# Kernel optimization log

Hardware: AMD Instinct MI355X
Metric: run time of the kernel (lower is better)

The kernel has to match this reference:

```python
import jax, jax.numpy as jnp
import numpy as np

B, N, C = 4, 2048, 1152
H = 16
DH = C // H  # 72
EPS = 1e-6
THETA = 10000.0


def _rms_norm(x, w):
    # per-head RMSNorm in fp32, matching LlamaRMSNorm
    xf = x.astype(jnp.float32)
    var = jnp.mean(xf * xf, axis=-1, keepdims=True)
    return (w * (xf * jax.lax.rsqrt(var + EPS)).astype(x.dtype))


def _rope_cos_sin(n, dh, dtype):
    half = dh // 2
    inv_freq = 1.0 / (THETA ** (jnp.arange(0, half, dtype=jnp.float32) / half))
    ang = jnp.arange(n, dtype=jnp.float32)[:, None] * inv_freq[None, :]  # [N, half]
    return jnp.cos(ang).astype(dtype), jnp.sin(ang).astype(dtype)


def _apply_rope(x, cos, sin):
    # x: [B,H,N,DH]; rotate-half style
    half = x.shape[-1] // 2
    x1, x2 = x[..., :half], x[..., half:]
    return jnp.concatenate([x1 * cos - x2 * sin, x2 * cos + x1 * sin], axis=-1)


def setup_inputs() -> dict:
    key = jax.random.key(0)
    ks = jax.random.split(key, 3)
    x = jax.random.normal(ks[0], (B, N, C), dtype=jnp.float32)
    w_qkv = jax.random.normal(ks[1], (3 * C, C), dtype=jnp.float32) * (C ** -0.5)
    w_proj = jax.random.normal(ks[2], (C, C), dtype=jnp.float32) * (C ** -0.5)
    b_proj = jnp.zeros((C,), dtype=jnp.float32)
    q_norm_w = jnp.ones((DH,), dtype=jnp.float32)
    k_norm_w = jnp.ones((DH,), dtype=jnp.float32)
    return {"x": x, "w_qkv": w_qkv, "w_proj": w_proj, "b_proj": b_proj,
            "q_norm_w": q_norm_w, "k_norm_w": k_norm_w}


def reference(x, w_qkv, w_proj, b_proj, q_norm_w, k_norm_w):
    b, n, c = x.shape
    # QKV projection (no bias)
    qkv = jnp.einsum('bnc,dc->bnd', x, w_qkv)  # [B,N,3C]
    qkv = qkv.reshape(b, n, 3, H, DH).transpose(2, 0, 3, 1, 4)  # [3,B,H,N,DH]
    q, k, v = qkv[0], qkv[1], qkv[2]
    # RoPE on q, k
    cos, sin = _rope_cos_sin(n, DH, x.dtype)  # [N, DH/2]
    q = _apply_rope(q, cos, sin)
    k = _apply_rope(k, cos, sin)
    # per-head QK RMSNorm
    q = _rms_norm(q, q_norm_w)
    k = _rms_norm(k, k_norm_w)
    # scaled dot-product attention
    scale = DH ** -0.5
    attn = jax.nn.softmax(jnp.einsum('bhqd,bhkd->bhqk', q, k) * scale, axis=-1)
    out = jnp.einsum('bhqk,bhkd->bhqd', attn, v)  # [B,H,N,DH]
    out = out.transpose(0, 2, 1, 3).reshape(b, n, c)
    return jnp.einsum('bnc,dc->bnd', out, w_proj) + b_proj
```

## Files before the change

kernel.cpp:

```cpp
#include <hip/hip_runtime.h>
#include <stdint.h>

#define BATCH 4
#define NSEQ  2048
#define CDIM  1152
#define HB    16
#define DHD   72
#define D3    3456
#define NT    8192

typedef __attribute__((ext_vector_type(8))) short short8;
typedef __attribute__((ext_vector_type(8))) unsigned short u16x8;
typedef __attribute__((ext_vector_type(4))) unsigned short u16x4;
typedef __attribute__((ext_vector_type(2))) unsigned int u32x2;
typedef __attribute__((ext_vector_type(4))) float f32x4;

__device__ __forceinline__ float bf2f(unsigned short u) {
  return __uint_as_float(((unsigned)u) << 16);
}
__device__ __forceinline__ unsigned short f2bf(float f) {
  unsigned u = __float_as_uint(f);
  u += 0x7FFF + ((u >> 16) & 1);
  return (unsigned short)(u >> 16);
}
__device__ __forceinline__ unsigned pkbf(float lo, float hi) {
  unsigned r;
  asm("v_cvt_pk_bf16_f32 %0, %1, %2" : "=v"(r) : "v"(lo), "v"(hi));
  return r;
}

__device__ __forceinline__ void gload_lds16(const unsigned short* g, unsigned short* l) {
  __builtin_amdgcn_global_load_lds(
      (const __attribute__((address_space(1))) void*)g,
      (__attribute__((address_space(3))) void*)l, 16, 0, 0);
}

#define XN    ((size_t)NT * CDIM)
#define WQN   ((size_t)D3 * CDIM)
#define WPN   ((size_t)CDIM * CDIM)
#define CVT_CHUNKS ((XN + WQN + WPN) / 4)

__global__ __launch_bounds__(256) void cvt_bf16(
    const float* __restrict__ x, const float* __restrict__ wq,
    const float* __restrict__ wp, unsigned short* __restrict__ xb,
    unsigned short* __restrict__ wqb, unsigned short* __restrict__ wpb) {
  size_t c = (size_t)blockIdx.x * 256 + threadIdx.x;
  if (c >= CVT_CHUNKS) return;
  const float* src;
  unsigned short* dst;
  size_t e = c * 4;
  if (e < XN) { src = x + e; dst = xb + e; }
  else if (e < XN + WQN) { src = wq + (e - XN); dst = wqb + (e - XN); }
  else { src = wp + (e - XN - WQN); dst = wpb + (e - XN - WQN); }
  f32x4 v = *(const f32x4*)src;
  u16x4 r;
#pragma unroll
  for (int i = 0; i < 4; i++) r[i] = f2bf(v[i]);
  *(u16x4*)dst = r;
}

template <int SCATTER>
__global__ __launch_bounds__(256) void gemm_bt(
    const unsigned short* __restrict__ A, const unsigned short* __restrict__ Bt,
    const float* __restrict__ bias, void* __restrict__ Cout,
    unsigned short* __restrict__ Vt, int M, int Dn, int K) {
  __shared__ __attribute__((aligned(16))) unsigned short sA[128 * 32];
  __shared__ __attribute__((aligned(16))) unsigned short sB[128 * 32];

  const int tid  = threadIdx.x;
  const int lane = tid & 63;
  const int w    = tid >> 6;
  const int wm   = w >> 1, wn = w & 1;
  const int quad = lane >> 4, l16 = lane & 15;

  const int gx  = gridDim.x;
  const int nwg = gx * gridDim.y;
  const int lb  = blockIdx.y * gx + blockIdx.x;
  const int swz = (lb & 7) * (nwg >> 3) + (lb >> 3);
  const int m0 = (swz / gx) * 128, n0 = (swz % gx) * 128;

  const int srow = (lane >> 2);
  const int scol = (lane & 3) << 3;

  const f32x4 zero = {0.f, 0.f, 0.f, 0.f};
  f32x4 acc[4][4];
#pragma unroll
  for (int i = 0; i < 4; i++)
#pragma unroll
    for (int j = 0; j < 4; j++) acc[i][j] = zero;

  for (int kt = 0; kt < K; kt += 32) {
#pragma unroll
    for (int i = 0; i < 2; i++) {
      int ck = w * 2 + i;
      gload_lds16(A + (size_t)(m0 + ck * 16 + srow) * K + kt + scol, sA + ck * 512);
      gload_lds16(Bt + (size_t)(n0 + ck * 16 + srow) * K + kt + scol, sB + ck * 512);
    }
    __syncthreads();

    short8 a[4], b[4];
#pragma unroll
    for (int i = 0; i < 4; i++)
      a[i] = *(const short8*)(sA + (wm * 64 + i * 16 + l16) * 32 + quad * 8);
#pragma unroll
    for (int j = 0; j < 4; j++)
      b[j] = *(const short8*)(sB + (wn * 64 + j * 16 + l16) * 32 + quad * 8);

#pragma unroll
    for (int i = 0; i < 4; i++)
#pragma unroll
      for (int j = 0; j < 4; j++)
        acc[i][j] = __builtin_amdgcn_mfma_f32_16x16x32_bf16(a[i], b[j], acc[i][j], 0, 0, 0);
    __syncthreads();
  }

#pragma unroll
  for (int i = 0; i < 4; i++) {
    int row = m0 + wm * 64 + i * 16 + quad * 4;
#pragma unroll
    for (int j = 0; j < 4; j++) {
      int col = n0 + wn * 64 + j * 16 + l16;
      if (SCATTER) {
        int s  = col / CDIM;
        int rm = col - s * CDIM;
        int h  = rm / DHD;
        int dh = rm - h * DHD;
        int b_ = row >> 11;
        int n  = row & 2047;
        if (s == 2) {
#pragma unroll
          for (int r = 0; r < 4; r++)
            Vt[((size_t)(b_ * HB + h) * DHD + dh) * NSEQ + n + r] = f2bf(acc[i][j][r]);
        } else {
          unsigned short* Cb = (unsigned short*)Cout;
#pragma unroll
          for (int r = 0; r < 4; r++)
            Cb[(((size_t)(s * BATCH + b_) * HB + h) * NSEQ + (n + r)) * DHD + dh] =
                f2bf(acc[i][j][r]);
        }
      } else {
        float bb = bias ? bias[col] : 0.f;
        float* Cf = (float*)Cout;
#pragma unroll
        for (int r = 0; r < 4; r++)
          Cf[(size_t)(row + r) * Dn + col] = acc[i][j][r] + bb;
      }
    }
  }
}

__global__ __launch_bounds__(256) void rope_rms(
    unsigned short* __restrict__ qkvb,
    const float* __restrict__ qw, const float* __restrict__ kw) {
  const int blk = blockIdx.x;
  const int b = blk >> 11;
  const int n = blk & 2047;
  const int tid = threadIdx.x;

  __shared__ float sv[2][CDIM];
  __shared__ float srsq[2][HB];

  const float nf = (float)n;
  const float l2t_over_half = 13.287712379549449f / 36.0f;
  const float scale2 = 0.17002329230297715f;

  for (int e = tid; e < CDIM; e += 256) {
    int h  = e / DHD;
    int dh = e - h * DHD;
    int i  = (dh < 36) ? dh : dh - 36;
    float inv_freq = exp2f(-l2t_over_half * (float)i);
    float ang = nf * inv_freq;
    float sn, cs;
    __sincosf(ang, &sn, &cs);
#pragma unroll
    for (int sel = 0; sel < 2; sel++) {
      size_t ah = (((size_t)(sel * BATCH + b) * HB + h) * NSEQ + n) * DHD;
      float x1 = bf2f(qkvb[ah + i]);
      float x2 = bf2f(qkvb[ah + i + 36]);
      sv[sel][e] = (dh < 36) ? (x1 * cs - x2 * sn) : (x2 * cs + x1 * sn);
    }
  }
  __syncthreads();
  if (tid < 128) {
    int sel = tid >> 6;
    int h = (tid & 63) >> 2, p = tid & 3;
    float s = 0.f;
#pragma unroll
    for (int d = 0; d < 18; d++) {
      float v = sv[sel][h * DHD + p * 18 + d];
      s += v * v;
    }
    s += __shfl_xor(s, 1);
    s += __shfl_xor(s, 2);
    if (p == 0)
      srsq[sel][h] = rsqrtf(s * (1.0f / 72.0f) + 1e-6f) * (sel ? 1.0f : scale2);
  }
  __syncthreads();
  for (int e = tid; e < CDIM; e += 256) {
    int h  = e / DHD;
    int dh = e - h * DHD;
#pragma unroll
    for (int sel = 0; sel < 2; sel++) {
      const float* wnorm = sel ? kw : qw;
      size_t ah = (((size_t)(sel * BATCH + b) * HB + h) * NSEQ + n) * DHD;
      qkvb[ah + dh] = f2bf(sv[sel][e] * srsq[sel][h] * wnorm[dh]);
    }
  }
}

__global__ __launch_bounds__(256, 4) void flash_attn(
    const unsigned short* __restrict__ qkvb, const unsigned short* __restrict__ Vt,
    unsigned short* __restrict__ AO) {
  __shared__ __attribute__((aligned(16))) unsigned short sK[64 * 72];
  __shared__ __attribute__((aligned(16))) unsigned short sVt[80 * 64];
  __shared__ __attribute__((aligned(16))) unsigned short sP[128 * 64];

  const int tid  = threadIdx.x;
  const int w    = tid >> 6;
  const int lane = tid & 63;
  const int quad = lane >> 4, l16 = lane & 15;
  const int s7   = l16 & 7;
  const int q0 = blockIdx.x * 128;
  const int h = blockIdx.y, b = blockIdx.z;

  const unsigned short* Qb = qkvb + ((size_t)(0 * BATCH + b) * HB + h) * NSEQ * DHD;
  const unsigned short* Kb = qkvb + ((size_t)(1 * BATCH + b) * HB + h) * NSEQ * DHD;
  const unsigned short* Vb = Vt + (size_t)(b * HB + h) * DHD * NSEQ;

  const short8 zs = {0, 0, 0, 0, 0, 0, 0, 0};
  const f32x4 zero = {0.f, 0.f, 0.f, 0.f};

  const int vswz = ((lane & 7) ^ (lane >> 3)) * 8;
  const unsigned short* pKn[3];
  const unsigned short* pVn[3];
#pragma unroll
  for (int j = 0; j < 3; j++) {
    int i = w + 4 * j;
    int ii = (i < 9) ? i : 0;
    pKn[j] = Kb + ii * 512 + lane * 8;
    pVn[j] = Vb + (size_t)(ii * 8 + (lane >> 3)) * NSEQ + vswz;
  }

#pragma unroll
  for (int j = 0; j < 3; j++) {
    int i = w + 4 * j;
    if (i < 9) {
      gload_lds16(pKn[j], sK + i * 512);
      gload_lds16(pVn[j], sVt + i * 512);
      pKn[j] += 64 * 72;
      pVn[j] += 64;
    }
  }

  for (int e = tid; e < 512; e += 256)
    sVt[72 * 64 + e] = (e < 64) ? (unsigned short)0x3F80 : (unsigned short)0;

  short8 aq[2][3];
#pragma unroll
  for (int qt = 0; qt < 2; qt++) {
    const unsigned short* qrow = Qb + (size_t)(q0 + w * 32 + qt * 16 + l16) * DHD;
    aq[qt][0] = *(const short8*)(qrow + quad * 8);
    aq[qt][1] = *(const short8*)(qrow + 32 + quad * 8);
    aq[qt][2] = (quad == 0) ? *(const short8*)(qrow + 64) : zs;
  }

  f32x4 o[2][5];
#pragma unroll
  for (int qt = 0; qt < 2; qt++)
#pragma unroll
    for (int nb = 0; nb < 5; nb++) o[qt][nb] = zero;

  auto sphase_pack = [&]() {
    f32x4 st[2][4];
    __builtin_amdgcn_s_setprio(1);
#pragma unroll
    for (int nk = 0; nk < 4; nk++) {
      const unsigned short* kr = sK + (nk * 16 + l16) * 72;
      short8 kf0 = *(const short8*)(kr + quad * 8);
      short8 kf1 = *(const short8*)(kr + 32 + quad * 8);
      short8 kf2 = *(const short8*)(kr + 64);
      f32x4 s0 = zero, s1 = zero;
      s0 = __builtin_amdgcn_mfma_f32_16x16x32_bf16(kf0, aq[0][0], s0, 0, 0, 0);
      s1 = __builtin_amdgcn_mfma_f32_16x16x32_bf16(kf0, aq[1][0], s1, 0, 0, 0);
      s0 = __builtin_amdgcn_mfma_f32_16x16x32_bf16(kf1, aq[0][1], s0, 0, 0, 0);
      s1 = __builtin_amdgcn_mfma_f32_16x16x32_bf16(kf1, aq[1][1], s1, 0, 0, 0);
      s0 = __builtin_amdgcn_mfma_f32_16x16x32_bf16(kf2, aq[0][2], s0, 0, 0, 0);
      s1 = __builtin_amdgcn_mfma_f32_16x16x32_bf16(kf2, aq[1][2], s1, 0, 0, 0);
      st[0][nk] = s0;
      st[1][nk] = s1;
    }
    __builtin_amdgcn_s_setprio(0);
#pragma unroll
    for (int qt = 0; qt < 2; qt++) {
      unsigned short* prow = sP + (qt * 64 + w * 16 + l16) * 64 + (quad & 1) * 4;
#pragma unroll
      for (int nk = 0; nk < 4; nk++) {
        int uoff = ((nk * 2 + (quad >> 1)) ^ s7) << 3;
        u32x2 pr;
        pr[0] = pkbf(exp2f(st[qt][nk][0]), exp2f(st[qt][nk][1]));
        pr[1] = pkbf(exp2f(st[qt][nk][2]), exp2f(st[qt][nk][3]));
        *(u32x2*)(prow + uoff) = pr;
      }
    }
  };

  auto pv_phase = [&]() {
    __builtin_amdgcn_s_setprio(1);
#pragma unroll
    for (int kb = 0; kb < 2; kb++) {
      const unsigned short* pp =
          sP + (w * 16 + l16) * 64 + (((kb * 4 + quad) ^ s7) << 3);
      short8 pf0 = *(const short8*)pp;
      short8 pf1 = *(const short8*)(pp + 64 * 64);
#pragma unroll
      for (int nb = 0; nb < 5; nb++) {
        short8 vf = *(const short8*)(sVt + (nb * 16 + l16) * 64 +
                                     (((kb * 4 + quad) ^ s7) << 3));
        o[0][nb] = __builtin_amdgcn_mfma_f32_16x16x32_bf16(pf0, vf, o[0][nb], 0, 0, 0);
        o[1][nb] = __builtin_amdgcn_mfma_f32_16x16x32_bf16(pf1, vf, o[1][nb], 0, 0, 0);
      }
    }
    __builtin_amdgcn_s_setprio(0);
  };

  __syncthreads();

  for (int t = 0; t < 32; t++) {
    sphase_pack();

    __syncthreads();

    if (t < 31) {
#pragma unroll
      for (int j = 0; j < 3; j++) {
        int i = w + 4 * j;
        if (i < 9) { gload_lds16(pKn[j], sK + i * 512); pKn[j] += 64 * 72; }
      }
    }

    pv_phase();

    __syncthreads();

    if (t < 31) {
#pragma unroll
      for (int j = 0; j < 3; j++) {
        int i = w + 4 * j;
        if (i < 9) { gload_lds16(pVn[j], sVt + i * 512); pVn[j] += 64; }
      }
    }
  }

#pragma unroll
  for (int qt = 0; qt < 2; qt++) {
    float inv[4];
#pragma unroll
    for (int r = 0; r < 4; r++)
      inv[r] = 1.0f / __shfl(o[qt][4][r], (quad << 4) + 8, 64);
    const int qrow = q0 + w * 32 + qt * 16 + quad * 4;
#pragma unroll
    for (int nb = 0; nb < 5; nb++) {
      int dh = nb * 16 + l16;
      if (dh < DHD) {
#pragma unroll
        for (int r = 0; r < 4; r++)
          AO[((size_t)b * NSEQ + qrow + r) * CDIM + h * DHD + dh] =
              f2bf(o[qt][nb][r] * inv[r]);
      }
    }
  }
}

extern "C" void kernel_launch(void* const* d_in, const int* in_sizes, int n_in,
                              void* d_out, int out_size, void* d_ws, size_t ws_size,
                              hipStream_t stream) {
  const float* x      = (const float*)d_in[0];
  const float* w_qkv  = (const float*)d_in[1];
  const float* w_proj = (const float*)d_in[2];
  const float* b_proj = (const float*)d_in[3];
  const float* qnw    = (const float*)d_in[4];
  const float* knw    = (const float*)d_in[5];
  float* out = (float*)d_out;

  char* ws = (char*)d_ws;
  unsigned short* xb    = (unsigned short*)(ws);
  unsigned short* wqkvb = (unsigned short*)(ws + 18874368);
  unsigned short* wprojb= (unsigned short*)(ws + 26836992);
  unsigned short* qkvb  = (unsigned short*)(ws + 29491200);
  unsigned short* Vt    = (unsigned short*)(ws + 67239936);
  unsigned short* AO    = xb;

  cvt_bf16<<<dim3((CVT_CHUNKS + 255) / 256), 256, 0, stream>>>(
      x, w_qkv, w_proj, xb, wqkvb, wprojb);
  gemm_bt<1><<<dim3(D3 / 128, NT / 128), 256, 0, stream>>>(
      xb, wqkvb, nullptr, qkvb, Vt, NT, D3, CDIM);
  rope_rms<<<dim3(NT), 256, 0, stream>>>(qkvb, qnw, knw);
  flash_attn<<<dim3(NSEQ / 128, HB, BATCH), 256, 0, stream>>>(qkvb, Vt, AO);
  gemm_bt<0><<<dim3(CDIM / 128, NT / 128), 256, 0, stream>>>(
      AO, wprojb, b_proj, out, nullptr, NT, CDIM, CDIM);
}
```

Measured before the change: 393.8 us.

## Deepen GEMM K-tile with XOR-swizzled LDS and vectorize rope_rms memory access

```diff
diff --git a/kernel.cpp b/kernel.cpp
--- a/kernel.cpp
+++ b/kernel.cpp
@@ -64,23 +64,27 @@
     const unsigned short* __restrict__ A, const unsigned short* __restrict__ Bt,
     const float* __restrict__ bias, void* __restrict__ Cout,
     unsigned short* __restrict__ Vt, int M, int Dn, int K) {
-  __shared__ __attribute__((aligned(16))) unsigned short sA[128 * 32];
-  __shared__ __attribute__((aligned(16))) unsigned short sB[128 * 32];
+  __shared__ __attribute__((aligned(16))) unsigned short sA[128 * 64];
+  __shared__ __attribute__((aligned(16))) unsigned short sB[128 * 64];
 
   const int tid  = threadIdx.x;
   const int lane = tid & 63;
   const int w    = tid >> 6;
   const int wm   = w >> 1, wn = w & 1;
   const int quad = lane >> 4, l16 = lane & 15;
+  const int s7l  = l16 & 7;
 
   const int gx  = gridDim.x;
-  const int nwg = gx * gridDim.y;
   const int lb  = blockIdx.y * gx + blockIdx.x;
-  const int swz = (lb & 7) * (nwg >> 3) + (lb >> 3);
-  const int m0 = (swz / gx) * 128, n0 = (swz % gx) * 128;
-
-  const int srow = (lane >> 2);
-  const int scol = (lane & 3) << 3;
+  const int xcd = lb & 7;
+  const int pos = lb >> 3;
+  const int m0 = ((xcd << 3) + (pos & 7)) * 128;
+  const int n0 = (pos >> 3) * 128;
+
+  const int r8 = lane >> 3;
+  const int cu = (lane & 7) ^ r8;
+  const unsigned short* gA = A  + (size_t)(m0 + w * 32 + r8) * K + cu * 8;
+  const unsigned short* gB = Bt + (size_t)(n0 + w * 32 + r8) * K + cu * 8;
 
   const f32x4 zero = {0.f, 0.f, 0.f, 0.f};
   f32x4 acc[4][4];
@@ -89,28 +93,30 @@
 #pragma unroll
     for (int j = 0; j < 4; j++) acc[i][j] = zero;
 
-  for (int kt = 0; kt < K; kt += 32) {
-#pragma unroll
-    for (int i = 0; i < 2; i++) {
-      int ck = w * 2 + i;
-      gload_lds16(A + (size_t)(m0 + ck * 16 + srow) * K + kt + scol, sA + ck * 512);
-      gload_lds16(Bt + (size_t)(n0 + ck * 16 + srow) * K + kt + scol, sB + ck * 512);
+  for (int kt = 0; kt < K; kt += 64) {
+#pragma unroll
+    for (int i = 0; i < 4; i++) {
+      gload_lds16(gA + (size_t)i * 8 * K + kt, sA + (w * 4 + i) * 512);
+      gload_lds16(gB + (size_t)i * 8 * K + kt, sB + (w * 4 + i) * 512);
     }
     __syncthreads();
 
-    short8 a[4], b[4];
-#pragma unroll
-    for (int i = 0; i < 4; i++)
-      a[i] = *(const short8*)(sA + (wm * 64 + i * 16 + l16) * 32 + quad * 8);
-#pragma unroll
-    for (int j = 0; j < 4; j++)
-      b[j] = *(const short8*)(sB + (wn * 64 + j * 16 + l16) * 32 + quad * 8);
-
-#pragma unroll
-    for (int i = 0; i < 4; i++)
-#pragma unroll
-      for (int j = 0; j < 4; j++)
-        acc[i][j] = __builtin_amdgcn_mfma_f32_16x16x32_bf16(a[i], b[j], acc[i][j], 0, 0, 0);
+#pragma unroll
+    for (int kk = 0; kk < 2; kk++) {
+      short8 a[4], b[4];
+#pragma unroll
+      for (int i = 0; i < 4; i++) {
+        a[i] = *(const short8*)(sA + (wm * 64 + i * 16 + l16) * 64 +
+                                (((kk * 4 + quad) ^ s7l) << 3));
+        b[i] = *(const short8*)(sB + (wn * 64 + i * 16 + l16) * 64 +
+                                (((kk * 4 + quad) ^ s7l) << 3));
+      }
+#pragma unroll
+      for (int i = 0; i < 4; i++)
+#pragma unroll
+        for (int j = 0; j < 4; j++)
+          acc[i][j] = __builtin_amdgcn_mfma_f32_16x16x32_bf16(a[i], b[j], acc[i][j], 0, 0, 0);
+    }
     __syncthreads();
   }
 
@@ -164,23 +170,35 @@
   const float l2t_over_half = 13.287712379549449f / 36.0f;
   const float scale2 = 0.17002329230297715f;
 
-  for (int e = tid; e < CDIM; e += 256) {
-    int h  = e / DHD;
-    int dh = e - h * DHD;
-    int i  = (dh < 36) ? dh : dh - 36;
-    float inv_freq = exp2f(-l2t_over_half * (float)i);
-    float ang = nf * inv_freq;
+  for (int g = tid; g < 288; g += 256) {
+    int sel = (g >= 144) ? 1 : 0;
+    int gg  = g - sel * 144;
+    int h   = gg / 9;
+    int u   = gg - h * 9;
+    const unsigned short* src =
+        qkvb + (((size_t)(sel * BATCH + b) * HB + h) * NSEQ + n) * DHD + u * 8;
+    u16x8 v = *(const u16x8*)src;
+    float* dst = &sv[sel][h * DHD + u * 8];
+#pragma unroll
+    for (int r = 0; r < 8; r++) dst[r] = bf2f(v[r]);
+  }
+  __syncthreads();
+
+  for (int p = tid; p < 1152; p += 256) {
+    int sel = (p >= 576) ? 1 : 0;
+    int pp  = p - sel * 576;
+    int h   = pp / 36;
+    int i   = pp - h * 36;
+    float* row = &sv[sel][h * DHD];
+    float x1 = row[i], x2 = row[i + 36];
+    float ang = nf * exp2f(-l2t_over_half * (float)i);
     float sn, cs;
     __sincosf(ang, &sn, &cs);
-#pragma unroll
-    for (int sel = 0; sel < 2; sel++) {
-      size_t ah = (((size_t)(sel * BATCH + b) * HB + h) * NSEQ + n) * DHD;
-      float x1 = bf2f(qkvb[ah + i]);
-      float x2 = bf2f(qkvb[ah + i + 36]);
-      sv[sel][e] = (dh < 36) ? (x1 * cs - x2 * sn) : (x2 * cs + x1 * sn);
-    }
+    row[i]      = x1 * cs - x2 * sn;
+    row[i + 36] = x2 * cs + x1 * sn;
   }
   __syncthreads();
+
   if (tid < 128) {
     int sel = tid >> 6;
     int h = (tid & 63) >> 2, p = tid & 3;
@@ -196,15 +214,21 @@
       srsq[sel][h] = rsqrtf(s * (1.0f / 72.0f) + 1e-6f) * (sel ? 1.0f : scale2);
   }
   __syncthreads();
-  for (int e = tid; e < CDIM; e += 256) {
-    int h  = e / DHD;
-    int dh = e - h * DHD;
-#pragma unroll
-    for (int sel = 0; sel < 2; sel++) {
-      const float* wnorm = sel ? kw : qw;
-      size_t ah = (((size_t)(sel * BATCH + b) * HB + h) * NSEQ + n) * DHD;
-      qkvb[ah + dh] = f2bf(sv[sel][e] * srsq[sel][h] * wnorm[dh]);
-    }
+
+  for (int g = tid; g < 288; g += 256) {
+    int sel = (g >= 144) ? 1 : 0;
+    int gg  = g - sel * 144;
+    int h   = gg / 9;
+    int u   = gg - h * 9;
+    float rs = srsq[sel][h];
+    const float* wn = (sel ? kw : qw) + u * 8;
+    const float* s = &sv[sel][h * DHD + u * 8];
+    u16x8 o;
+#pragma unroll
+    for (int r = 0; r < 8; r++) o[r] = f2bf(s[r] * rs * wn[r]);
+    unsigned short* dst =
+        qkvb + (((size_t)(sel * BATCH + b) * HB + h) * NSEQ + n) * DHD + u * 8;
+    *(u16x8*)dst = o;
   }
 }
 
```

New measurement: 367.6 us. -6.7%, faster.
